# Kernel tuning notes

Measured on AMD Instinct MI355X. Metric: run time of the kernel, lower is better.

Reference implementation:

```python
import jax, jax.numpy as jnp
import numpy as np

N_USERS = 100_000
N_ITEMS = 150_000
N_REL = 16
N_FACT = 4
D = 64
N_EDGES = 2_000_000
NNZ = 2_000_000
N_LAYERS = 2


def setup_inputs() -> dict:
    key = jax.random.key(0)
    ks = jax.random.split(key, 10)
    return {
        "user_emb": jax.random.normal(ks[0], (N_USERS, D), jnp.float32) * 0.1,
        "entity_emb": jax.random.normal(ks[1], (N_ITEMS, D), jnp.float32) * 0.1,
        "latent_emb": jax.random.normal(ks[2], (N_FACT, D), jnp.float32) * 0.1,
        "weight": jax.random.normal(ks[3], (N_REL, D), jnp.float32) * 0.1,
        "disen_weight_att": jax.random.normal(ks[4], (N_FACT, N_REL), jnp.float32) * 0.1,
        "interact_val": jax.random.uniform(ks[5], (NNZ,), jnp.float32),
        "edge_index": jax.random.randint(ks[6], (2, N_EDGES), 0, N_ITEMS),
        "edge_type": jax.random.randint(ks[7], (N_EDGES,), 1, N_REL + 1),
        "interact_row": jax.random.randint(ks[8], (NNZ,), 0, N_USERS),
        "interact_col": jax.random.randint(ks[9], (NNZ,), 0, N_ITEMS),
    }


def _dist_corr(t1, t2):
    # torch _distance_correlation on 1-D vectors of length n
    n = t1.shape[0]
    t1 = t1[:, None]
    t2 = t2[:, None]
    dx = jnp.sqrt(jnp.maximum(t1 ** 2 - 2.0 * (t1 @ t1.T) + (t1 ** 2).T, 0.0) + 1e-8)
    dy = jnp.sqrt(jnp.maximum(t2 ** 2 - 2.0 * (t2 @ t2.T) + (t2 ** 2).T, 0.0) + 1e-8)
    A = dx - dx.mean(0, keepdims=True) - dx.mean(1, keepdims=True) + dx.mean()
    B = dy - dy.mean(0, keepdims=True) - dy.mean(1, keepdims=True) + dy.mean()
    dcov = lambda P, Q: jnp.sqrt(jnp.maximum((P * Q).sum() / (n * n), 0.0) + 1e-8)
    return dcov(A, B) / jnp.sqrt(dcov(A, A) * dcov(B, B) + 1e-8)


def _l2_normalize(x):
    # F.normalize(x) default: dim=1, eps=1e-12
    nrm = jnp.sqrt(jnp.sum(x * x, axis=1, keepdims=True))
    return x / jnp.maximum(nrm, 1e-12)


def _forward(user_emb, entity_emb, latent_emb, weight, disen_weight_att,
             interact_val, edge_index, edge_type, interact_row, interact_col):
    head, tail = edge_index[0], edge_index[1]
    entity_res, user_res = entity_emb, user_emb

    # correlation score over disentangled factor pairs (n_factors small, fixed loop)
    cor = jnp.asarray(0.0, jnp.float32)
    for i in range(N_FACT):
        for j in range(i + 1, N_FACT):
            cor = cor + _dist_corr(disen_weight_att[i], disen_weight_att[j])

    ones_e = jnp.ones((N_EDGES,), entity_emb.dtype)
    cnt = jax.ops.segment_sum(ones_e, head, num_segments=N_ITEMS)  # [n_items]
    denom = jnp.maximum(cnt, 1.0)[:, None]

    for _ in range(N_LAYERS):
        # KG aggregate: gather + elementwise mul + scatter_mean
        msg = entity_emb[tail] * weight[edge_type - 1]            # [E, D]
        entity_agg = jax.ops.segment_sum(msg, head, num_segments=N_ITEMS) / denom

        # user->factor attention
        score = jax.nn.softmax(user_emb @ latent_emb.T, axis=1)[..., None]  # [U, F, 1]

        # sparse mm: user_agg = interact_mat @ entity_emb
        user_agg = jax.ops.segment_sum(interact_val[:, None] * entity_emb[interact_col],
                                       interact_row, num_segments=N_USERS)  # [U, D]

        dis = jax.nn.softmax(disen_weight_att, axis=-1) @ weight  # [F, D]
        mix = (dis[None, :, :] * score).sum(axis=1)               # [U, D]
        user_agg = user_agg * mix + user_agg

        entity_emb = _l2_normalize(entity_agg)
        user_emb = _l2_normalize(user_agg)
        entity_res = entity_res + entity_emb
        user_res = user_res + user_emb

    return entity_res, user_res, cor


def reference(user_emb, entity_emb, latent_emb, weight, disen_weight_att,
              interact_val, edge_index, edge_type, interact_row, interact_col):
    return _forward(user_emb, entity_emb, latent_emb, weight, disen_weight_att,
                    interact_val, edge_index, edge_type, interact_row, interact_col)
```

## Files before the change

### kernel.cpp

```cpp
#include <hip/hip_runtime.h>

#define N_USERS 100000
#define N_ITEMS 150000
#define N_REL 16
#define N_FACT 4
#define DD 64
#define N_EDGES 2000000
#define NNZ 2000000

#define KE 293
#define KU 196
#define TBE 4096
#define TBU 2048
#define GEB ((N_EDGES + TBE - 1) / TBE)
#define GUB ((NNZ + TBU - 1) / TBU)
#define EBLK2 ((N_ITEMS + 31) / 32)
#define UBLK2 (N_USERS / 32)
#define CAPE 8192
#define CAPU 12288

typedef float          __attribute__((ext_vector_type(4))) f32x4;
typedef unsigned short __attribute__((ext_vector_type(8))) u16x8;

__device__ __forceinline__ unsigned short f2b(float f) {
    unsigned u = __float_as_uint(f);
    return (unsigned short)((u + 0x7FFFu + ((u >> 16) & 1u)) >> 16);
}
__device__ __forceinline__ float b2f(unsigned short h) {
    return __uint_as_float((unsigned)h << 16);
}


__global__ __launch_bounds__(256) void init_kernel(const float4* __restrict__ uemb,
                                                   const float4* __restrict__ eemb,
                                                   ushort4* __restrict__ entB0_u4,
                                                   float4* __restrict__ cur_usr,
                                                   float4* __restrict__ eres,
                                                   float4* __restrict__ ures,
                                                   int* __restrict__ bktcntE,
                                                   int* __restrict__ bktcntU) {
    int i = blockIdx.x * 256 + threadIdx.x;
    const int NE4 = N_ITEMS * 16;
    const int NU4 = N_USERS * 16;
    if (i < NE4) {
        float4 v = eemb[i];
        eres[i] = v;
        int rr = i >> 4, f = i & 15;
        entB0_u4[(size_t)rr * 16 + ((f & 7) << 1) + (f >> 3)] =
            make_ushort4(f2b(v.x), f2b(v.y), f2b(v.z), f2b(v.w));
    }
    if (i < NU4) { float4 v = uemb[i]; cur_usr[i] = v; ures[i] = v; }
    if (i < KE) bktcntE[i] = 0;
    if (i < KU) bktcntU[i] = 0;
}

__global__ __launch_bounds__(256) void small_kernel(const float* __restrict__ att,
                                                    const float* __restrict__ weight,
                                                    float* __restrict__ cor_out,
                                                    float* __restrict__ dis) {
    __shared__ float sA[256], sB[256];
    __shared__ float srx[16], scx[16], sry[16], scy[16];
    __shared__ float stotx, stoty;
    int t = threadIdx.x;
    if (blockIdx.x == 1) {
        int f = t >> 6, d = t & 63;
        float m = -1e30f;
        for (int r = 0; r < N_REL; ++r) m = fmaxf(m, att[f * N_REL + r]);
        float w[N_REL]; float s = 0.f;
        for (int r = 0; r < N_REL; ++r) { w[r] = expf(att[f * N_REL + r] - m); s += w[r]; }
        float acc = 0.f;
        for (int r = 0; r < N_REL; ++r) acc += (w[r] / s) * weight[r * DD + d];
        dis[f * DD + d] = acc;
        return;
    }
    int a = t >> 4, b = t & 15;
    float cor_acc = 0.f;
    for (int i = 0; i < N_FACT; ++i) {
        for (int j = i + 1; j < N_FACT; ++j) {
            const float* t1 = att + i * N_REL;
            const float* t2 = att + j * N_REL;
            float d1 = t1[a] - t1[b];
            float d2 = t2[a] - t2[b];
            float dx = sqrtf(d1 * d1 + 1e-8f);
            float dy = sqrtf(d2 * d2 + 1e-8f);
            sA[t] = dx; sB[t] = dy;
            __syncthreads();
            if (t < 16)      { float s = 0; for (int k = 0; k < 16; ++k) s += sA[t * 16 + k]; srx[t] = s; }
            else if (t < 32) { int c = t & 15; float s = 0; for (int k = 0; k < 16; ++k) s += sA[k * 16 + c]; scx[c] = s; }
            else if (t < 48) { int r = t & 15; float s = 0; for (int k = 0; k < 16; ++k) s += sB[r * 16 + k]; sry[r] = s; }
            else if (t < 64) { int c = t & 15; float s = 0; for (int k = 0; k < 16; ++k) s += sB[k * 16 + c]; scy[c] = s; }
            __syncthreads();
            if (t == 0)  { float s = 0; for (int k = 0; k < 16; ++k) s += srx[k]; stotx = s; }
            if (t == 64) { float s = 0; for (int k = 0; k < 16; ++k) s += sry[k]; stoty = s; }
            __syncthreads();
            float A = dx - scx[b] * 0.0625f - srx[a] * 0.0625f + stotx * (1.f / 256.f);
            float B = dy - scy[b] * 0.0625f - sry[a] * 0.0625f + stoty * (1.f / 256.f);
            float vab = A * B, vaa = A * A, vbb = B * B;
            for (int off = 32; off; off >>= 1) {
                vab += __shfl_xor(vab, off, 64);
                vaa += __shfl_xor(vaa, off, 64);
                vbb += __shfl_xor(vbb, off, 64);
            }
            __syncthreads();
            if ((t & 63) == 0) {
                int w = t >> 6;
                sA[w] = vab; sA[4 + w] = vaa; sA[8 + w] = vbb;
            }
            __syncthreads();
            if (t == 0) {
                float sAB = sA[0] + sA[1] + sA[2] + sA[3];
                float sAA = sA[4] + sA[5] + sA[6] + sA[7];
                float sBB = sA[8] + sA[9] + sA[10] + sA[11];
                float dab = sqrtf(fmaxf(sAB * (1.f / 256.f), 0.f) + 1e-8f);
                float daa = sqrtf(fmaxf(sAA * (1.f / 256.f), 0.f) + 1e-8f);
                float dbb = sqrtf(fmaxf(sBB * (1.f / 256.f), 0.f) + 1e-8f);
                cor_acc += dab / sqrtf(daa * dbb + 1e-8f);
            }
            __syncthreads();
        }
    }
    if (t == 0) *cor_out = cor_acc;
}

struct BinSME {
    unsigned int stage[TBE];
    unsigned short sbkt[TBE];
    int hist[KE];
    int lofs[KE + 1];
    int gbase[KE];
};
struct BinSMU {
    unsigned long long stage[TBU];
    unsigned short sbkt[TBU];
    int hist[KU];
    int lofs[KU + 1];
    int gbase[KU];
};
__global__ __launch_bounds__(256) void bin_both_kernel(const int* __restrict__ eidx,
                                                       const int* __restrict__ etype,
                                                       const int* __restrict__ irow,
                                                       const int* __restrict__ icol,
                                                       const float* __restrict__ ival,
                                                       int* __restrict__ bktcntE,
                                                       int* __restrict__ bktcntU,
                                                       unsigned int* __restrict__ binE,
                                                       unsigned long long* __restrict__ binU) {
    __shared__ union { BinSME e; BinSMU u; } sm;
    int tid = threadIdx.x;
    if (blockIdx.x < GEB) {
        int e0 = blockIdx.x * TBE;
        int nloc = min(TBE, N_EDGES - e0);
        for (int b = tid; b < KE; b += 256) sm.e.hist[b] = 0;
        __syncthreads();
        for (int i = tid; i < nloc; i += 256)
            atomicAdd(&sm.e.hist[__builtin_nontemporal_load(&eidx[e0 + i]) >> 9], 1);
        __syncthreads();
        if (tid < 64) {
            const int chunk = (KE + 63) >> 6;
            int base = tid * chunk;
            int s = 0;
            for (int c = 0; c < chunk; ++c) { int ix = base + c; if (ix < KE) s += sm.e.hist[ix]; }
            int inc = s;
            for (int d = 1; d < 64; d <<= 1) { int tv = __shfl_up(inc, d, 64); if (tid >= d) inc += tv; }
            int run = inc - s;
            for (int c = 0; c < chunk; ++c) { int ix = base + c; if (ix < KE) { sm.e.lofs[ix] = run; run += sm.e.hist[ix]; } }
            if (tid == 63) sm.e.lofs[KE] = run;
        }
        __syncthreads();
        for (int b = tid; b < KE; b += 256) {
            int cnt = sm.e.lofs[b + 1] - sm.e.lofs[b];
            if (cnt > 0) sm.e.gbase[b] = atomicAdd(&bktcntE[b], cnt);
            sm.e.hist[b] = sm.e.lofs[b];
        }
        __syncthreads();
        for (int i = tid; i < nloc; i += 256) {
            int h = __builtin_nontemporal_load(&eidx[e0 + i]);
            int tt = __builtin_nontemporal_load(&eidx[N_EDGES + e0 + i]);
            int r  = __builtin_nontemporal_load(&etype[e0 + i]) - 1;
            int b = h >> 9;
            int slot = atomicAdd(&sm.e.hist[b], 1);
            sm.e.stage[slot] = (unsigned int)tt | ((unsigned int)r << 18) | ((unsigned int)(h & 511) << 22);
            sm.e.sbkt[slot] = (unsigned short)b;
        }
        __syncthreads();
        int total = sm.e.lofs[KE];
        for (int i = tid; i < total; i += 256) {
            int b = sm.e.sbkt[i];
            int slot = sm.e.gbase[b] + (i - sm.e.lofs[b]);
            if (slot < CAPE) binE[(size_t)b * CAPE + slot] = sm.e.stage[i];
        }
    } else {
        int e0 = (blockIdx.x - GEB) * TBU;
        int nloc = min(TBU, NNZ - e0);
        for (int b = tid; b < KU; b += 256) sm.u.hist[b] = 0;
        __syncthreads();
        for (int i = tid; i < nloc; i += 256)
            atomicAdd(&sm.u.hist[__builtin_nontemporal_load(&irow[e0 + i]) >> 9], 1);
        __syncthreads();
        if (tid < 64) {
            const int chunk = (KU + 63) >> 6;
            int base = tid * chunk;
            int s = 0;
            for (int c = 0; c < chunk; ++c) { int ix = base + c; if (ix < KU) s += sm.u.hist[ix]; }
            int inc = s;
            for (int d = 1; d < 64; d <<= 1) { int tv = __shfl_up(inc, d, 64); if (tid >= d) inc += tv; }
            int run = inc - s;
            for (int c = 0; c < chunk; ++c) { int ix = base + c; if (ix < KU) { sm.u.lofs[ix] = run; run += sm.u.hist[ix]; } }
            if (tid == 63) sm.u.lofs[KU] = run;
        }
        __syncthreads();
        for (int b = tid; b < KU; b += 256) {
            int cnt = sm.u.lofs[b + 1] - sm.u.lofs[b];
            if (cnt > 0) sm.u.gbase[b] = atomicAdd(&bktcntU[b], cnt);
            sm.u.hist[b] = sm.u.lofs[b];
        }
        __syncthreads();
        for (int i = tid; i < nloc; i += 256) {
            int row = __builtin_nontemporal_load(&irow[e0 + i]);
            int col = __builtin_nontemporal_load(&icol[e0 + i]);
            float v  = __builtin_nontemporal_load(&ival[e0 + i]);
            int b = row >> 9;
            int slot = atomicAdd(&sm.u.hist[b], 1);
            sm.u.stage[slot] = ((unsigned long long)__float_as_uint(v) << 32)
                             | ((unsigned long long)(row & 511) << 18)
                             | (unsigned int)col;
            sm.u.sbkt[slot] = (unsigned short)b;
        }
        __syncthreads();
        int total = sm.u.lofs[KU];
        for (int i = tid; i < total; i += 256) {
            int b = sm.u.sbkt[i];
            int slot = sm.u.gbase[b] + (i - sm.u.lofs[b]);
            if (slot < CAPU) binU[(size_t)b * CAPU + slot] = sm.u.stage[i];
        }
    }
}

__global__ __launch_bounds__(512) void bucket_scan_kernel(const int* __restrict__ bktcntE,
                                                          const int* __restrict__ bktcntU,
                                                          int* __restrict__ bbaseE,
                                                          int* __restrict__ bbaseU,
                                                          int* __restrict__ eoff,
                                                          int* __restrict__ uoff) {
    __shared__ int lds[512];
    int t = threadIdx.x;
    const int* cnt; int* bbase; int K; int* off; int n; int cap;
    if (blockIdx.x == 0) { cnt = bktcntE; bbase = bbaseE; K = KE; off = eoff; n = N_ITEMS; cap = CAPE; }
    else                 { cnt = bktcntU; bbase = bbaseU; K = KU; off = uoff; n = N_USERS; cap = CAPU; }
    int v = (t < K) ? min(cnt[t], cap) : 0;
    lds[t] = v; __syncthreads();
    for (int o = 1; o < 512; o <<= 1) {
        int add = (t >= o) ? lds[t - o] : 0;
        __syncthreads();
        lds[t] += add;
        __syncthreads();
    }
    if (t < K) bbase[t] = lds[t] - v;
    if (t == K - 1) off[n] = lds[t];
}

__global__ __launch_bounds__(256) void fine_both_kernel(const int* __restrict__ bktcntE,
                                                        const int* __restrict__ bktcntU,
                                                        const int* __restrict__ bbaseE,
                                                        const int* __restrict__ bbaseU,
                                                        const unsigned int* __restrict__ binE,
                                                        const unsigned long long* __restrict__ binU,
                                                        int* __restrict__ eoff,
                                                        int* __restrict__ uoff,
                                                        int* __restrict__ pack,
                                                        unsigned long long* __restrict__ upair) {
    __shared__ int hist[512];
    __shared__ int scanb[256];
    __shared__ int curs[512];
    int tid = threadIdx.x;
    if (blockIdx.x < KE) {
        int b = blockIdx.x;
        int row0 = b << 9;
        int cnt = min(bktcntE[b], CAPE);
        int base = bbaseE[b];
        for (int r = tid; r < 512; r += 256) hist[r] = 0;
        __syncthreads();
        for (int i = tid; i < cnt; i += 256)
            atomicAdd(&hist[binE[(size_t)b * CAPE + i] >> 22], 1);
        __syncthreads();
        int a0 = hist[2 * tid], a1 = hist[2 * tid + 1];
        int s = a0 + a1;
        scanb[tid] = s; __syncthreads();
        for (int o = 1; o < 256; o <<= 1) {
            int add = (tid >= o) ? scanb[tid - o] : 0;
            __syncthreads();
            scanb[tid] += add;
            __syncthreads();
        }
        int excl = scanb[tid] - s;
        curs[2 * tid]     = base + excl;
        curs[2 * tid + 1] = base + excl + a0;
        int row = row0 + 2 * tid;
        if (row < N_ITEMS)     eoff[row]     = base + excl;
        if (row + 1 < N_ITEMS) eoff[row + 1] = base + excl + a0;
        __syncthreads();
        for (int i = tid; i < cnt; i += 256) {
            unsigned int p = binE[(size_t)b * CAPE + i];
            int pos = atomicAdd(&curs[p >> 22], 1);
            pack[pos] = (int)(p & 0x3FFFFF);
        }
    } else {
        int b = blockIdx.x - KE;
        int row0 = b << 9;
        int cnt = min(bktcntU[b], CAPU);
        int base = bbaseU[b];
        for (int r = tid; r < 512; r += 256) hist[r] = 0;
        __syncthreads();
        for (int i = tid; i < cnt; i += 256)
            atomicAdd(&hist[(int)(binU[(size_t)b * CAPU + i] >> 18) & 511], 1);
        __syncthreads();
        int a0 = hist[2 * tid], a1 = hist[2 * tid + 1];
        int s = a0 + a1;
        scanb[tid] = s; __syncthreads();
        for (int o = 1; o < 256; o <<= 1) {
            int add = (tid >= o) ? scanb[tid - o] : 0;
            __syncthreads();
            scanb[tid] += add;
            __syncthreads();
        }
        int excl = scanb[tid] - s;
        curs[2 * tid]     = base + excl;
        curs[2 * tid + 1] = base + excl + a0;
        int row = row0 + 2 * tid;
        if (row < N_USERS)     uoff[row]     = base + excl;
        if (row + 1 < N_USERS) uoff[row + 1] = base + excl + a0;
        __syncthreads();
        for (int i = tid; i < cnt; i += 256) {
            unsigned long long p = binU[(size_t)b * CAPU + i];
            int pos = atomicAdd(&curs[(int)(p >> 18) & 511], 1);
            upair[pos] = p & 0xFFFFFFFF0003FFFFull;
        }
    }
}

__global__ __launch_bounds__(256) void layer_kernel(const int* __restrict__ eoff,
                                                    const int* __restrict__ pack,
                                                    const int* __restrict__ uoff,
                                                    const unsigned long long* __restrict__ upair,
                                                    const u16x8* __restrict__ entBIn,
                                                    const float4* __restrict__ w4,
                                                    const float4* __restrict__ lat4,
                                                    const float4* __restrict__ dis4,
                                                    u16x8* __restrict__ entBOut,
                                                    float4* __restrict__ eres4,
                                                    float4* __restrict__ usr4,
                                                    float4* __restrict__ ures4) {
    int w = threadIdx.x >> 6;
    int lane = threadIdx.x & 63;
    int g = lane >> 3, li = lane & 7;
    if (blockIdx.x < EBLK2) {
        int row = blockIdx.x * 32 + w * 8 + g;
        bool valid = row < N_ITEMS;
        int beg = 0, deg = 0;
        if (valid) { beg = eoff[row]; deg = eoff[row + 1] - beg; }
        int mdeg = deg;
        for (int o = 8; o < 64; o <<= 1) mdeg = max(mdeg, __shfl_xor(mdeg, o, 64));
        float4 a0 = make_float4(0.f, 0.f, 0.f, 0.f);
        float4 a1 = make_float4(0.f, 0.f, 0.f, 0.f);
        for (int cb = 0; cb < mdeg; cb += 8) {
            int pk = 0;
            if (cb + li < deg) pk = __builtin_nontemporal_load(&pack[beg + cb + li]);
            int pv[8];
            #pragma unroll
            for (int k = 0; k < 8; ++k) pv[k] = __shfl(pk, k, 8);
            u16x8 rows[8];
            #pragma unroll
            for (int k = 0; k < 8; ++k)
                rows[k] = entBIn[(size_t)(pv[k] & 0x3FFFF) * 8 + li];
            #pragma unroll
            for (int k = 0; k < 8; ++k) {
                if (cb + k < deg) {
                    int r = pv[k] >> 18;
                    float4 wa = w4[r * 16 + li];
                    float4 wb = w4[r * 16 + 8 + li];
                    a0.x += b2f(rows[k][0]) * wa.x; a0.y += b2f(rows[k][1]) * wa.y;
                    a0.z += b2f(rows[k][2]) * wa.z; a0.w += b2f(rows[k][3]) * wa.w;
                    a1.x += b2f(rows[k][4]) * wb.x; a1.y += b2f(rows[k][5]) * wb.y;
                    a1.z += b2f(rows[k][6]) * wb.z; a1.w += b2f(rows[k][7]) * wb.w;
                }
            }
        }
        if (valid) {
            float inv = 1.f / fmaxf((float)deg, 1.f);
            a0.x *= inv; a0.y *= inv; a0.z *= inv; a0.w *= inv;
            a1.x *= inv; a1.y *= inv; a1.z *= inv; a1.w *= inv;
            float ss = a0.x * a0.x + a0.y * a0.y + a0.z * a0.z + a0.w * a0.w
                     + a1.x * a1.x + a1.y * a1.y + a1.z * a1.z + a1.w * a1.w;
            for (int o = 4; o; o >>= 1) ss += __shfl_xor(ss, o, 8);
            float rn = 1.f / fmaxf(sqrtf(ss), 1e-12f);
            a0.x *= rn; a0.y *= rn; a0.z *= rn; a0.w *= rn;
            a1.x *= rn; a1.y *= rn; a1.z *= rn; a1.w *= rn;
            u16x8 ob;
            ob[0] = f2b(a0.x); ob[1] = f2b(a0.y); ob[2] = f2b(a0.z); ob[3] = f2b(a0.w);
            ob[4] = f2b(a1.x); ob[5] = f2b(a1.y); ob[6] = f2b(a1.z); ob[7] = f2b(a1.w);
            entBOut[(size_t)row * 8 + li] = ob;
            float4 r0 = eres4[(size_t)row * 16 + li];
            float4 r1 = eres4[(size_t)row * 16 + 8 + li];
            r0.x += a0.x; r0.y += a0.y; r0.z += a0.z; r0.w += a0.w;
            r1.x += a1.x; r1.y += a1.y; r1.z += a1.z; r1.w += a1.w;
            eres4[(size_t)row * 16 + li]     = r0;
            eres4[(size_t)row * 16 + 8 + li] = r1;
        }
    } else {
        int u = (blockIdx.x - EBLK2) * 32 + w * 8 + g;
        float4 uv0 = usr4[(size_t)u * 16 + li];
        float4 uv1 = usr4[(size_t)u * 16 + 8 + li];
        float p0, p1, p2, p3;
        {
            float4 la = lat4[0 * 16 + li], lb = lat4[0 * 16 + 8 + li];
            p0 = uv0.x * la.x + uv0.y * la.y + uv0.z * la.z + uv0.w * la.w
               + uv1.x * lb.x + uv1.y * lb.y + uv1.z * lb.z + uv1.w * lb.w;
        }
        {
            float4 la = lat4[1 * 16 + li], lb = lat4[1 * 16 + 8 + li];
            p1 = uv0.x * la.x + uv0.y * la.y + uv0.z * la.z + uv0.w * la.w
               + uv1.x * lb.x + uv1.y * lb.y + uv1.z * lb.z + uv1.w * lb.w;
        }
        {
            float4 la = lat4[2 * 16 + li], lb = lat4[2 * 16 + 8 + li];
            p2 = uv0.x * la.x + uv0.y * la.y + uv0.z * la.z + uv0.w * la.w
               + uv1.x * lb.x + uv1.y * lb.y + uv1.z * lb.z + uv1.w * lb.w;
        }
        {
            float4 la = lat4[3 * 16 + li], lb = lat4[3 * 16 + 8 + li];
            p3 = uv0.x * la.x + uv0.y * la.y + uv0.z * la.z + uv0.w * la.w
               + uv1.x * lb.x + uv1.y * lb.y + uv1.z * lb.z + uv1.w * lb.w;
        }
        for (int o = 4; o; o >>= 1) {
            p0 += __shfl_xor(p0, o, 8);
            p1 += __shfl_xor(p1, o, 8);
            p2 += __shfl_xor(p2, o, 8);
            p3 += __shfl_xor(p3, o, 8);
        }
        float m = fmaxf(fmaxf(p0, p1), fmaxf(p2, p3));
        float e0 = expf(p0 - m), e1 = expf(p1 - m), e2 = expf(p2 - m), e3 = expf(p3 - m);
        float sinv = 1.f / (e0 + e1 + e2 + e3);
        float s0 = e0 * sinv, s1 = e1 * sinv, s2 = e2 * sinv, s3 = e3 * sinv;
        float4 mix0, mix1;
        {
            float4 d0a = dis4[0 * 16 + li], d1a = dis4[1 * 16 + li];
            float4 d2a = dis4[2 * 16 + li], d3a = dis4[3 * 16 + li];
            mix0 = make_float4(d0a.x * s0 + d1a.x * s1 + d2a.x * s2 + d3a.x * s3,
                               d0a.y * s0 + d1a.y * s1 + d2a.y * s2 + d3a.y * s3,
                               d0a.z * s0 + d1a.z * s1 + d2a.z * s2 + d3a.z * s3,
                               d0a.w * s0 + d1a.w * s1 + d2a.w * s2 + d3a.w * s3);
            float4 d0b = dis4[0 * 16 + 8 + li], d1b = dis4[1 * 16 + 8 + li];
            float4 d2b = dis4[2 * 16 + 8 + li], d3b = dis4[3 * 16 + 8 + li];
            mix1 = make_float4(d0b.x * s0 + d1b.x * s1 + d2b.x * s2 + d3b.x * s3,
                               d0b.y * s0 + d1b.y * s1 + d2b.y * s2 + d3b.y * s3,
                               d0b.z * s0 + d1b.z * s1 + d2b.z * s2 + d3b.z * s3,
                               d0b.w * s0 + d1b.w * s1 + d2b.w * s2 + d3b.w * s3);
        }
        int beg = uoff[u];
        int deg = uoff[u + 1] - beg;
        int mdeg = deg;
        for (int o = 8; o < 64; o <<= 1) mdeg = max(mdeg, __shfl_xor(mdeg, o, 64));
        float4 a0 = make_float4(0.f, 0.f, 0.f, 0.f);
        float4 a1 = make_float4(0.f, 0.f, 0.f, 0.f);
        for (int cb = 0; cb < mdeg; cb += 8) {
            unsigned long long pr = 0;
            if (cb + li < deg) pr = __builtin_nontemporal_load(&upair[beg + cb + li]);
            int clo[8]; float cval[8];
            #pragma unroll
            for (int k = 0; k < 8; ++k) {
                clo[k]  = __shfl((int)(pr & 0xFFFFFFFFu), k, 8);
                cval[k] = __uint_as_float((unsigned)__shfl((int)(pr >> 32), k, 8));
            }
            u16x8 rows[8];
            #pragma unroll
            for (int k = 0; k < 8; ++k)
                rows[k] = entBIn[(size_t)clo[k] * 8 + li];
            #pragma unroll
            for (int k = 0; k < 8; ++k) {
                float cv = cval[k];
                a0.x += cv * b2f(rows[k][0]); a0.y += cv * b2f(rows[k][1]);
                a0.z += cv * b2f(rows[k][2]); a0.w += cv * b2f(rows[k][3]);
                a1.x += cv * b2f(rows[k][4]); a1.y += cv * b2f(rows[k][5]);
                a1.z += cv * b2f(rows[k][6]); a1.w += cv * b2f(rows[k][7]);
            }
        }
        float4 v0 = make_float4(a0.x * mix0.x + a0.x, a0.y * mix0.y + a0.y,
                                a0.z * mix0.z + a0.z, a0.w * mix0.w + a0.w);
        float4 v1 = make_float4(a1.x * mix1.x + a1.x, a1.y * mix1.y + a1.y,
                                a1.z * mix1.z + a1.z, a1.w * mix1.w + a1.w);
        float ss = v0.x * v0.x + v0.y * v0.y + v0.z * v0.z + v0.w * v0.w
                 + v1.x * v1.x + v1.y * v1.y + v1.z * v1.z + v1.w * v1.w;
        for (int o = 4; o; o >>= 1) ss += __shfl_xor(ss, o, 8);
        float rn = 1.f / fmaxf(sqrtf(ss), 1e-12f);
        v0.x *= rn; v0.y *= rn; v0.z *= rn; v0.w *= rn;
        v1.x *= rn; v1.y *= rn; v1.z *= rn; v1.w *= rn;
        usr4[(size_t)u * 16 + li]     = v0;
        usr4[(size_t)u * 16 + 8 + li] = v1;
        float4 r0 = ures4[(size_t)u * 16 + li];
        float4 r1 = ures4[(size_t)u * 16 + 8 + li];
        r0.x += v0.x; r0.y += v0.y; r0.z += v0.z; r0.w += v0.w;
        r1.x += v1.x; r1.y += v1.y; r1.z += v1.z; r1.w += v1.w;
        ures4[(size_t)u * 16 + li]     = r0;
        ures4[(size_t)u * 16 + 8 + li] = r1;
    }
}

extern "C" void kernel_launch(void* const* d_in, const int* in_sizes, int n_in,
                              void* d_out, int out_size, void* d_ws, size_t ws_size,
                              hipStream_t stream) {
    const float* user_emb   = (const float*)d_in[0];
    const float* entity_emb = (const float*)d_in[1];
    const float* latent     = (const float*)d_in[2];
    const float* weight     = (const float*)d_in[3];
    const float* att        = (const float*)d_in[4];
    const float* ival       = (const float*)d_in[5];
    const int*   eidx       = (const int*)d_in[6];
    const int*   etype      = (const int*)d_in[7];
    const int*   irow       = (const int*)d_in[8];
    const int*   icol       = (const int*)d_in[9];

    float* out        = (float*)d_out;
    float* entity_res = out;
    float* user_res   = out + (size_t)N_ITEMS * DD;
    float* cor_out    = out + (size_t)N_ITEMS * DD + (size_t)N_USERS * DD;

    char* ws = (char*)d_ws;
    char* entB0 = ws;               ws += (size_t)N_ITEMS * DD * 2;
    char* entB1 = ws;               ws += (size_t)N_ITEMS * DD * 2;
    float* cur_usr = (float*)ws;    ws += (size_t)N_USERS * DD * 4;
    int*   eoff    = (int*)ws;      ws += (size_t)(N_ITEMS + 1) * 4;
    int*   epack   = (int*)ws;      ws += (size_t)N_EDGES * 4;
    int*   uoff    = (int*)ws;      ws += (size_t)(N_USERS + 1) * 4;
    unsigned long long* upair = (unsigned long long*)ws; ws += (size_t)NNZ * 8;
    unsigned long long* binU  = (unsigned long long*)ws; ws += (size_t)KU * CAPU * 8;
    int*   bktcntE = (int*)ws;      ws += 512 * 4;
    int*   bktcntU = (int*)ws;      ws += 512 * 4;
    int*   bbaseE  = (int*)ws;      ws += 512 * 4;
    int*   bbaseU  = (int*)ws;      ws += 512 * 4;
    float* dis     = (float*)ws;    ws += 256 * 4;
    unsigned int* binE = (unsigned int*)entB1;

    init_kernel<<<(N_ITEMS * 16 + 255) / 256, 256, 0, stream>>>(
        (const float4*)user_emb, (const float4*)entity_emb,
        (ushort4*)entB0, (float4*)cur_usr, (float4*)entity_res, (float4*)user_res,
        bktcntE, bktcntU);

    small_kernel<<<2, 256, 0, stream>>>(att, weight, cor_out, dis);

    bin_both_kernel<<<GEB + GUB, 256, 0, stream>>>(eidx, etype, irow, icol, ival,
                                                   bktcntE, bktcntU, binE, binU);
    bucket_scan_kernel<<<2, 512, 0, stream>>>(bktcntE, bktcntU, bbaseE, bbaseU, eoff, uoff);
    fine_both_kernel<<<KE + KU, 256, 0, stream>>>(bktcntE, bktcntU, bbaseE, bbaseU,
                                                  binE, binU, eoff, uoff, epack, upair);

    char* entbuf[2] = { entB0, entB1 };
    for (int layer = 0; layer < 2; ++layer) {
        char* eIn  = entbuf[layer & 1];
        char* eOut = entbuf[(layer & 1) ^ 1];
        layer_kernel<<<EBLK2 + UBLK2, 256, 0, stream>>>(eoff, epack, uoff, upair,
                                                        (const u16x8*)eIn,
                                                        (const float4*)weight,
                                                        (const float4*)latent,
                                                        (const float4*)dis,
                                                        (u16x8*)eOut,
                                                        (float4*)entity_res,
                                                        (float4*)cur_usr,
                                                        (float4*)user_res);
    }
}
```

Measured before the change: 371.5 us.

## Fuse init, small and binning kernels; make layer kernel persistent grid-stride

The init, small-statistics and binning kernels are merged into one prologue kernel that dispatches on block index, and the bucket counters are cleared with memsets instead. This cuts kernel launches and lets the independent prologue work run concurrently instead of in series. The layer kernel now runs a fixed grid of 2048 blocks that loop over entity and user tiles, which reduces block scheduling overhead. The risks are worse load balance across the persistent blocks and slightly higher shared memory use in the prologue.

```diff
diff --git a/kernel.cpp b/kernel.cpp
--- a/kernel.cpp
+++ b/kernel.cpp
@@ -16,6 +16,8 @@
 #define GUB ((NNZ + TBU - 1) / TBU)
 #define EBLK2 ((N_ITEMS + 31) / 32)
 #define UBLK2 (N_USERS / 32)
+#define LGRID 2048
+#define IBLK ((N_ITEMS * 16 + 255) / 256)
 #define CAPE 8192
 #define CAPU 12288
 
@@ -30,97 +32,6 @@
     return __uint_as_float((unsigned)h << 16);
 }
 
-
-__global__ __launch_bounds__(256) void init_kernel(const float4* __restrict__ uemb,
-                                                   const float4* __restrict__ eemb,
-                                                   ushort4* __restrict__ entB0_u4,
-                                                   float4* __restrict__ cur_usr,
-                                                   float4* __restrict__ eres,
-                                                   float4* __restrict__ ures,
-                                                   int* __restrict__ bktcntE,
-                                                   int* __restrict__ bktcntU) {
-    int i = blockIdx.x * 256 + threadIdx.x;
-    const int NE4 = N_ITEMS * 16;
-    const int NU4 = N_USERS * 16;
-    if (i < NE4) {
-        float4 v = eemb[i];
-        eres[i] = v;
-        int rr = i >> 4, f = i & 15;
-        entB0_u4[(size_t)rr * 16 + ((f & 7) << 1) + (f >> 3)] =
-            make_ushort4(f2b(v.x), f2b(v.y), f2b(v.z), f2b(v.w));
-    }
-    if (i < NU4) { float4 v = uemb[i]; cur_usr[i] = v; ures[i] = v; }
-    if (i < KE) bktcntE[i] = 0;
-    if (i < KU) bktcntU[i] = 0;
-}
-
-__global__ __launch_bounds__(256) void small_kernel(const float* __restrict__ att,
-                                                    const float* __restrict__ weight,
-                                                    float* __restrict__ cor_out,
-                                                    float* __restrict__ dis) {
-    __shared__ float sA[256], sB[256];
-    __shared__ float srx[16], scx[16], sry[16], scy[16];
-    __shared__ float stotx, stoty;
-    int t = threadIdx.x;
-    if (blockIdx.x == 1) {
-        int f = t >> 6, d = t & 63;
-        float m = -1e30f;
-        for (int r = 0; r < N_REL; ++r) m = fmaxf(m, att[f * N_REL + r]);
-        float w[N_REL]; float s = 0.f;
-        for (int r = 0; r < N_REL; ++r) { w[r] = expf(att[f * N_REL + r] - m); s += w[r]; }
-        float acc = 0.f;
-        for (int r = 0; r < N_REL; ++r) acc += (w[r] / s) * weight[r * DD + d];
-        dis[f * DD + d] = acc;
-        return;
-    }
-    int a = t >> 4, b = t & 15;
-    float cor_acc = 0.f;
-    for (int i = 0; i < N_FACT; ++i) {
-        for (int j = i + 1; j < N_FACT; ++j) {
-            const float* t1 = att + i * N_REL;
-            const float* t2 = att + j * N_REL;
-            float d1 = t1[a] - t1[b];
-            float d2 = t2[a] - t2[b];
-            float dx = sqrtf(d1 * d1 + 1e-8f);
-            float dy = sqrtf(d2 * d2 + 1e-8f);
-            sA[t] = dx; sB[t] = dy;
-            __syncthreads();
-            if (t < 16)      { float s = 0; for (int k = 0; k < 16; ++k) s += sA[t * 16 + k]; srx[t] = s; }
-            else if (t < 32) { int c = t & 15; float s = 0; for (int k = 0; k < 16; ++k) s += sA[k * 16 + c]; scx[c] = s; }
-            else if (t < 48) { int r = t & 15; float s = 0; for (int k = 0; k < 16; ++k) s += sB[r * 16 + k]; sry[r] = s; }
-            else if (t < 64) { int c = t & 15; float s = 0; for (int k = 0; k < 16; ++k) s += sB[k * 16 + c]; scy[c] = s; }
-            __syncthreads();
-            if (t == 0)  { float s = 0; for (int k = 0; k < 16; ++k) s += srx[k]; stotx = s; }
-            if (t == 64) { float s = 0; for (int k = 0; k < 16; ++k) s += sry[k]; stoty = s; }
-            __syncthreads();
-            float A = dx - scx[b] * 0.0625f - srx[a] * 0.0625f + stotx * (1.f / 256.f);
-            float B = dy - scy[b] * 0.0625f - sry[a] * 0.0625f + stoty * (1.f / 256.f);
-            float vab = A * B, vaa = A * A, vbb = B * B;
-            for (int off = 32; off; off >>= 1) {
-                vab += __shfl_xor(vab, off, 64);
-                vaa += __shfl_xor(vaa, off, 64);
-                vbb += __shfl_xor(vbb, off, 64);
-            }
-            __syncthreads();
-            if ((t & 63) == 0) {
-                int w = t >> 6;
-                sA[w] = vab; sA[4 + w] = vaa; sA[8 + w] = vbb;
-            }
-            __syncthreads();
-            if (t == 0) {
-                float sAB = sA[0] + sA[1] + sA[2] + sA[3];
-                float sAA = sA[4] + sA[5] + sA[6] + sA[7];
-                float sBB = sA[8] + sA[9] + sA[10] + sA[11];
-                float dab = sqrtf(fmaxf(sAB * (1.f / 256.f), 0.f) + 1e-8f);
-                float daa = sqrtf(fmaxf(sAA * (1.f / 256.f), 0.f) + 1e-8f);
-                float dbb = sqrtf(fmaxf(sBB * (1.f / 256.f), 0.f) + 1e-8f);
-                cor_acc += dab / sqrtf(daa * dbb + 1e-8f);
-            }
-            __syncthreads();
-        }
-    }
-    if (t == 0) *cor_out = cor_acc;
-}
 
 struct BinSME {
     unsigned int stage[TBE];
@@ -136,7 +47,18 @@
     int lofs[KU + 1];
     int gbase[KU];
 };
-__global__ __launch_bounds__(256) void bin_both_kernel(const int* __restrict__ eidx,
+
+__global__ __launch_bounds__(256) void prologue_kernel(const float4* __restrict__ uemb,
+                                                       const float4* __restrict__ eemb,
+                                                       ushort4* __restrict__ entB0_u4,
+                                                       float4* __restrict__ cur_usr,
+                                                       float4* __restrict__ eres,
+                                                       float4* __restrict__ ures,
+                                                       const float* __restrict__ att,
+                                                       const float* __restrict__ weight,
+                                                       float* __restrict__ cor_out,
+                                                       float* __restrict__ dis,
+                                                       const int* __restrict__ eidx,
                                                        const int* __restrict__ etype,
                                                        const int* __restrict__ irow,
                                                        const int* __restrict__ icol,
@@ -146,9 +68,13 @@
                                                        unsigned int* __restrict__ binE,
                                                        unsigned long long* __restrict__ binU) {
     __shared__ union { BinSME e; BinSMU u; } sm;
+    __shared__ float sA[256], sB[256];
+    __shared__ float srx[16], scx[16], sry[16], scy[16];
+    __shared__ float stotx, stoty;
     int tid = threadIdx.x;
-    if (blockIdx.x < GEB) {
-        int e0 = blockIdx.x * TBE;
+    int bid = blockIdx.x;
+    if (bid < GEB) {
+        int e0 = bid * TBE;
         int nloc = min(TBE, N_EDGES - e0);
         for (int b = tid; b < KE; b += 256) sm.e.hist[b] = 0;
         __syncthreads();
@@ -189,8 +115,8 @@
             int slot = sm.e.gbase[b] + (i - sm.e.lofs[b]);
             if (slot < CAPE) binE[(size_t)b * CAPE + slot] = sm.e.stage[i];
         }
-    } else {
-        int e0 = (blockIdx.x - GEB) * TBU;
+    } else if (bid < GEB + GUB) {
+        int e0 = (bid - GEB) * TBU;
         int nloc = min(TBU, NNZ - e0);
         for (int b = tid; b < KU; b += 256) sm.u.hist[b] = 0;
         __syncthreads();
@@ -233,6 +159,79 @@
             int slot = sm.u.gbase[b] + (i - sm.u.lofs[b]);
             if (slot < CAPU) binU[(size_t)b * CAPU + slot] = sm.u.stage[i];
         }
+    } else if (bid < GEB + GUB + 2) {
+        int sb = bid - (GEB + GUB);
+        int t = tid;
+        if (sb == 1) {
+            int f = t >> 6, d = t & 63;
+            float m = -1e30f;
+            for (int r = 0; r < N_REL; ++r) m = fmaxf(m, att[f * N_REL + r]);
+            float w[N_REL]; float s = 0.f;
+            for (int r = 0; r < N_REL; ++r) { w[r] = expf(att[f * N_REL + r] - m); s += w[r]; }
+            float acc = 0.f;
+            for (int r = 0; r < N_REL; ++r) acc += (w[r] / s) * weight[r * DD + d];
+            dis[f * DD + d] = acc;
+            return;
+        }
+        int a = t >> 4, b = t & 15;
+        float cor_acc = 0.f;
+        for (int i = 0; i < N_FACT; ++i) {
+            for (int j = i + 1; j < N_FACT; ++j) {
+                const float* t1 = att + i * N_REL;
+                const float* t2 = att + j * N_REL;
+                float d1 = t1[a] - t1[b];
+                float d2 = t2[a] - t2[b];
+                float dx = sqrtf(d1 * d1 + 1e-8f);
+                float dy = sqrtf(d2 * d2 + 1e-8f);
+                sA[t] = dx; sB[t] = dy;
+                __syncthreads();
+                if (t < 16)      { float s = 0; for (int k = 0; k < 16; ++k) s += sA[t * 16 + k]; srx[t] = s; }
+                else if (t < 32) { int c = t & 15; float s = 0; for (int k = 0; k < 16; ++k) s += sA[k * 16 + c]; scx[c] = s; }
+                else if (t < 48) { int r = t & 15; float s = 0; for (int k = 0; k < 16; ++k) s += sB[r * 16 + k]; sry[r] = s; }
+                else if (t < 64) { int c = t & 15; float s = 0; for (int k = 0; k < 16; ++k) s += sB[k * 16 + c]; scy[c] = s; }
+                __syncthreads();
+                if (t == 0)  { float s = 0; for (int k = 0; k < 16; ++k) s += srx[k]; stotx = s; }
+                if (t == 64) { float s = 0; for (int k = 0; k < 16; ++k) s += sry[k]; stoty = s; }
+                __syncthreads();
+                float A = dx - scx[b] * 0.0625f - srx[a] * 0.0625f + stotx * (1.f / 256.f);
+                float B = dy - scy[b] * 0.0625f - sry[a] * 0.0625f + stoty * (1.f / 256.f);
+                float vab = A * B, vaa = A * A, vbb = B * B;
+                for (int off = 32; off; off >>= 1) {
+                    vab += __shfl_xor(vab, off, 64);
+                    vaa += __shfl_xor(vaa, off, 64);
+                    vbb += __shfl_xor(vbb, off, 64);
+                }
+                __syncthreads();
+                if ((t & 63) == 0) {
+                    int w = t >> 6;
+                    sA[w] = vab; sA[4 + w] = vaa; sA[8 + w] = vbb;
+                }
+                __syncthreads();
+                if (t == 0) {
+                    float sAB = sA[0] + sA[1] + sA[2] + sA[3];
+                    float sAA = sA[4] + sA[5] + sA[6] + sA[7];
+                    float sBB = sA[8] + sA[9] + sA[10] + sA[11];
+                    float dab = sqrtf(fmaxf(sAB * (1.f / 256.f), 0.f) + 1e-8f);
+                    float daa = sqrtf(fmaxf(sAA * (1.f / 256.f), 0.f) + 1e-8f);
+                    float dbb = sqrtf(fmaxf(sBB * (1.f / 256.f), 0.f) + 1e-8f);
+                    cor_acc += dab / sqrtf(daa * dbb + 1e-8f);
+                }
+                __syncthreads();
+            }
+        }
+        if (t == 0) *cor_out = cor_acc;
+    } else {
+        int i = (bid - (GEB + GUB + 2)) * 256 + tid;
+        const int NE4 = N_ITEMS * 16;
+        const int NU4 = N_USERS * 16;
+        if (i < NE4) {
+            float4 v = eemb[i];
+            eres[i] = v;
+            int rr = i >> 4, f = i & 15;
+            entB0_u4[(size_t)rr * 16 + ((f & 7) << 1) + (f >> 3)] =
+                make_ushort4(f2b(v.x), f2b(v.y), f2b(v.z), f2b(v.w));
+        }
+        if (i < NU4) { float4 v = uemb[i]; cur_usr[i] = v; ures[i] = v; }
     }
 }
 
@@ -353,8 +352,9 @@
     int w = threadIdx.x >> 6;
     int lane = threadIdx.x & 63;
     int g = lane >> 3, li = lane & 7;
-    if (blockIdx.x < EBLK2) {
-        int row = blockIdx.x * 32 + w * 8 + g;
+    for (int tile = blockIdx.x; tile < EBLK2 + UBLK2; tile += LGRID) {
+    if (tile < EBLK2) {
+        int row = tile * 32 + w * 8 + g;
         bool valid = row < N_ITEMS;
         int beg = 0, deg = 0;
         if (valid) { beg = eoff[row]; deg = eoff[row + 1] - beg; }
@@ -407,7 +407,7 @@
             eres4[(size_t)row * 16 + 8 + li] = r1;
         }
     } else {
-        int u = (blockIdx.x - EBLK2) * 32 + w * 8 + g;
+        int u = (tile - EBLK2) * 32 + w * 8 + g;
         float4 uv0 = usr4[(size_t)u * 16 + li];
         float4 uv1 = usr4[(size_t)u * 16 + 8 + li];
         float p0, p1, p2, p3;
@@ -503,6 +503,7 @@
         ures4[(size_t)u * 16 + li]     = r0;
         ures4[(size_t)u * 16 + 8 + li] = r1;
     }
+    }
 }
 
 extern "C" void kernel_launch(void* const* d_in, const int* in_sizes, int n_in,
@@ -540,15 +541,16 @@
     float* dis     = (float*)ws;    ws += 256 * 4;
     unsigned int* binE = (unsigned int*)entB1;
 
-    init_kernel<<<(N_ITEMS * 16 + 255) / 256, 256, 0, stream>>>(
+    hipMemsetAsync(bktcntE, 0, 512 * 4, stream);
+    hipMemsetAsync(bktcntU, 0, 512 * 4, stream);
+
+    prologue_kernel<<<GEB + GUB + 2 + IBLK, 256, 0, stream>>>(
         (const float4*)user_emb, (const float4*)entity_emb,
         (ushort4*)entB0, (float4*)cur_usr, (float4*)entity_res, (float4*)user_res,
-        bktcntE, bktcntU);
-
-    small_kernel<<<2, 256, 0, stream>>>(att, weight, cor_out, dis);
-
-    bin_both_kernel<<<GEB + GUB, 256, 0, stream>>>(eidx, etype, irow, icol, ival,
-                                                   bktcntE, bktcntU, binE, binU);
+        att, weight, cor_out, dis,
+        eidx, etype, irow, icol, ival,
+        bktcntE, bktcntU, binE, binU);
+
     bucket_scan_kernel<<<2, 512, 0, stream>>>(bktcntE, bktcntU, bbaseE, bbaseU, eoff, uoff);
     fine_both_kernel<<<KE + KU, 256, 0, stream>>>(bktcntE, bktcntU, bbaseE, bbaseU,
                                                   binE, binU, eoff, uoff, epack, upair);
@@ -557,14 +559,14 @@
     for (int layer = 0; layer < 2; ++layer) {
         char* eIn  = entbuf[layer & 1];
         char* eOut = entbuf[(layer & 1) ^ 1];
-        layer_kernel<<<EBLK2 + UBLK2, 256, 0, stream>>>(eoff, epack, uoff, upair,
-                                                        (const u16x8*)eIn,
-                                                        (const float4*)weight,
-                                                        (const float4*)latent,
-                                                        (const float4*)dis,
-                                                        (u16x8*)eOut,
-                                                        (float4*)entity_res,
-                                                        (float4*)cur_usr,
-                                                        (float4*)user_res);
+        layer_kernel<<<LGRID, 256, 0, stream>>>(eoff, epack, uoff, upair,
+                                                (const u16x8*)eIn,
+                                                (const float4*)weight,
+                                                (const float4*)latent,
+                                                (const float4*)dis,
+                                                (u16x8*)eOut,
+                                                (float4*)entity_res,
+                                                (float4*)cur_usr,
+                                                (float4*)user_res);
     }
 }
```

New measurement: 387.9 us. 4.4% more time.
